# Kernel optimization log

Measured on AMD Instinct MI355X. Metric: run time of the kernel, lower is better.

The kernel has to match this reference:

```python
import jax, jax.numpy as jnp
import numpy as np

NUM_HEADS = 16
HEAD_DIM = 128
ROT_DIM = 128  # rotary_emb_dim == head_dim
ROPE_BASE = 10000.0


def setup_inputs() -> dict:
    key = jax.random.key(0)
    k1, k2, k3, k4, k5 = jax.random.split(key, 5)
    b, s, d = 2, 2048, 2048
    return {
        "x": jax.random.normal(k1, (b, s, d), jnp.float32),
        "Wqkv_w": jax.random.normal(k2, (3 * d, d), jnp.float32) * (d ** -0.5),
        "Wqkv_b": jax.random.normal(k3, (3 * d,), jnp.float32) * 0.02,
        "wo_w": jax.random.normal(k4, (d, d), jnp.float32) * (d ** -0.5),
        "wo_b": jax.random.normal(k5, (d,), jnp.float32) * 0.02,
    }


def _deinterleave(t):
    # torch.cat([t[..., ::2], t[..., 1::2]], dim=-1)
    return jnp.concatenate([t[..., ::2], t[..., 1::2]], axis=-1)


def _rope(t, cos, sin):
    # non-interleaved (GPT-NeoX style) rotary on first ROT_DIM dims; here ROT_DIM == head_dim
    half = ROT_DIM // 2
    x1, x2 = t[..., :half], t[..., half:ROT_DIM]
    # cos/sin: (s, half) -> broadcast over (b, s, h, half)
    c = cos[None, :, None, :]
    sn = sin[None, :, None, :]
    return jnp.concatenate([x1 * c - x2 * sn, x2 * c + x1 * sn], axis=-1)


def reference(x, Wqkv_w, Wqkv_b, wo_w, wo_b):
    b, s, d = x.shape
    h, hd = NUM_HEADS, HEAD_DIM
    # fused QKV projection, layout '(h three d)' per original rearrange
    qkv = x @ Wqkv_w.T + Wqkv_b                      # (b, s, 3*d)
    qkv = qkv.reshape(b, s, h, 3, hd)
    q = _deinterleave(qkv[:, :, :, 0, :])            # (b, s, h, hd)
    k = _deinterleave(qkv[:, :, :, 1, :])
    v = qkv[:, :, :, 2, :]
    # rotary embedding tables
    inv_freq = 1.0 / (ROPE_BASE ** (jnp.arange(0, ROT_DIM, 2, dtype=jnp.float32) / ROT_DIM))
    freqs = jnp.arange(s, dtype=jnp.float32)[:, None] * inv_freq[None, :]  # (s, half)
    cos, sin = jnp.cos(freqs), jnp.sin(freqs)
    q = _rope(q, cos, sin)
    k = _rope(k, cos, sin)
    # causal self-attention (SelfAttention, softmax_scale = 1/sqrt(hd))
    scale = hd ** -0.5
    scores = jnp.einsum('bshd,bthd->bhst', q, k) * scale  # (b, h, s, s)
    mask = jnp.tril(jnp.ones((s, s), dtype=bool))
    scores = jnp.where(mask[None, None], scores, jnp.finfo(scores.dtype).min)
    probs = jax.nn.softmax(scores, axis=-1)
    ctx = jnp.einsum('bhst,bthd->bshd', probs, v)    # (b, s, h, hd)
    ctx = ctx.reshape(b, s, d)
    return ctx @ wo_w.T + wo_b
```

## Files before the change

kernel.cpp:

```cpp
#include <hip/hip_runtime.h>

#define B_ 2
#define S_ 2048
#define H_ 16
#define HD_ 128
#define QKVROW 6144
#define M_ 4096

typedef float f32x4 __attribute__((ext_vector_type(4)));
typedef __bf16 bf16x8 __attribute__((ext_vector_type(8)));
typedef unsigned short ushortx8 __attribute__((ext_vector_type(8)));

__device__ __forceinline__ float bf2f(unsigned short u) {
  union { unsigned u; float f; } v;
  v.u = ((unsigned)u) << 16;
  return v.f;
}
__device__ __forceinline__ unsigned short f2bf(float f) {
  union { __bf16 b; unsigned short u; } c;
  c.b = (__bf16)f;
  return c.u;
}
__device__ __forceinline__ ushortx8 cvt8(const float* f) {
  const f32x4 lo = *(const f32x4*)f;
  const f32x4 hi = *(const f32x4*)(f + 4);
  ushortx8 o;
#pragma unroll
  for (int t = 0; t < 4; ++t) o[t] = f2bf(lo[t]);
#pragma unroll
  for (int t = 0; t < 4; ++t) o[4 + t] = f2bf(hi[t]);
  return o;
}
__device__ __forceinline__ void async16(const unsigned short* g, unsigned short* l) {
  __builtin_amdgcn_global_load_lds(
      (const __attribute__((address_space(1))) unsigned int*)g,
      (__attribute__((address_space(3))) unsigned int*)l, 16, 0, 0);
}

__global__ __launch_bounds__(256) void f2bf3t(
    const float* __restrict__ a, unsigned short* __restrict__ da, int na8,
    const float* __restrict__ b, unsigned short* __restrict__ db, int nb8,
    const float* __restrict__ c, unsigned short* __restrict__ dc, int nc8,
    float* __restrict__ tab, int nt8) {
  const int ntot = na8 + nb8 + nc8 + nt8;
  int i = blockIdx.x * 256 + threadIdx.x;
  const int stride = gridDim.x * 256;
  for (; i < ntot; i += stride) {
    int off = i;
    if (off < na8 + nb8 + nc8) {
      const float* s;
      unsigned short* d;
      if (off < na8) { s = a; d = da; }
      else if (off - na8 < nb8) { off -= na8; s = b; d = db; }
      else { off -= na8 + nb8; s = c; d = dc; }
      const ushortx8 o = cvt8(s + (size_t)off * 8);
      *(ushortx8*)&d[(size_t)off * 8] = o;
    } else {
      off -= na8 + nb8 + nc8;
      float* dt = tab + (size_t)off * 8;
      const int e0 = off * 8;
      const int s = e0 >> 7;
#pragma unroll
      for (int k = 0; k < 4; ++k) {
        const int j = ((e0 & 127) >> 1) + k;
        const float invf = expf(-(float)j * 0.14391156831212787f);
        float sn, cs;
        sincosf((float)s * invf, &sn, &cs);
        dt[2 * k] = cs;
        dt[2 * k + 1] = sn;
      }
    }
  }
}

__global__ __launch_bounds__(256) void gemm1(
    const unsigned short* __restrict__ A, const unsigned short* __restrict__ Bm,
    const float* __restrict__ bias, unsigned short* __restrict__ C) {
  __shared__ unsigned short As[128 * 64];
  __shared__ unsigned short Bs[128 * 64];
  const int tid = threadIdx.x;
  const int lane = tid & 63, wave = tid >> 6;
  const int l15 = lane & 15, quad = lane >> 4;
  const int m0 = blockIdx.y * 128, n0 = blockIdx.x * 128;
  const int wr = (wave >> 1) * 64, wc = (wave & 1) * 64;

  f32x4 acc[4][4];
#pragma unroll
  for (int r = 0; r < 4; ++r)
#pragma unroll
    for (int c = 0; c < 4; ++c) acc[r][c] = (f32x4){0.f, 0.f, 0.f, 0.f};

  for (int k0 = 0; k0 < 2048; k0 += 64) {
    __syncthreads();
#pragma unroll
    for (int i = 0; i < 4; ++i) {
      const int c0 = wave * 256 + i * 64;
      const int u = c0 + lane;
      const int row = u >> 3, cu = u & 7;
      const int cs = cu ^ (row & 7);
      async16(A + (size_t)(m0 + row) * 2048 + k0 + cs * 8, &As[c0 * 8]);
      async16(Bm + (size_t)(n0 + row) * 2048 + k0 + cs * 8, &Bs[c0 * 8]);
    }
    __syncthreads();

#pragma unroll
    for (int s = 0; s < 2; ++s) {
      bf16x8 af[4], bf[4];
#pragma unroll
      for (int r = 0; r < 4; ++r) {
        const int row = wr + r * 16 + l15;
        af[r] = *(const bf16x8*)&As[row * 64 + (((s * 4 + quad) ^ (row & 7)) << 3)];
      }
#pragma unroll
      for (int c = 0; c < 4; ++c) {
        const int row = wc + c * 16 + l15;
        bf[c] = *(const bf16x8*)&Bs[row * 64 + (((s * 4 + quad) ^ (row & 7)) << 3)];
      }
#pragma unroll
      for (int r = 0; r < 4; ++r)
#pragma unroll
        for (int c = 0; c < 4; ++c)
          acc[r][c] = __builtin_amdgcn_mfma_f32_16x16x32_bf16(af[r], bf[c], acc[r][c], 0, 0, 0);
    }
  }

#pragma unroll
  for (int c = 0; c < 4; ++c) {
    const int col = n0 + wc + c * 16 + l15;
    const float bv = bias[col];
#pragma unroll
    for (int r = 0; r < 4; ++r) {
      const int row = m0 + wr + r * 16 + quad * 4;
#pragma unroll
      for (int i = 0; i < 4; ++i)
        C[(size_t)(row + i) * QKVROW + col] = f2bf(acc[r][c][i] + bv);
    }
  }
}

__global__ __launch_bounds__(256) void rope_vt(
    unsigned short* qkv, unsigned short* __restrict__ Vt,
    const float* __restrict__ tab) {
  __shared__ unsigned short vs[64 * 136];
  const int b = blockIdx.z, h = blockIdx.y, s0 = blockIdx.x * 64;
  const int tid = threadIdx.x;
  const int r = tid >> 2, cpart = (tid & 3) * 32;
  const int s = s0 + r;
  unsigned short* base = qkv + (size_t)(b * S_ + s) * QKVROW + h * 384;
  const int j0 = cpart >> 1;

  ushortx8 ivq[4], ivk[4], ivv[4];
#pragma unroll
  for (int i = 0; i < 4; ++i) {
    ivq[i] = *(const ushortx8*)&base[cpart + i * 8];
    ivk[i] = *(const ushortx8*)&base[128 + cpart + i * 8];
    ivv[i] = *(const ushortx8*)&base[256 + cpart + i * 8];
  }

  float cs[16], sn[16];
  {
    const f32x4* tr = (const f32x4*)&tab[(size_t)s * 128 + j0 * 2];
#pragma unroll
    for (int t = 0; t < 8; ++t) {
      const f32x4 v = tr[t];
      cs[2 * t] = v[0]; sn[2 * t] = v[1];
      cs[2 * t + 1] = v[2]; sn[2 * t + 1] = v[3];
    }
  }

  __syncthreads();

#pragma unroll
  for (int which = 0; which < 2; ++which) {
    const ushortx8* iv = (which == 0) ? ivq : ivk;
    const float scale =
        (which == 0) ? (0.08838834764831845f * 1.4426950408889634f) : 1.0f;
    ushortx8 o1a, o1b, o2a, o2b;
#pragma unroll
    for (int t = 0; t < 16; ++t) {
      const float x1 = bf2f(iv[(2 * t) >> 3][(2 * t) & 7]);
      const float x2 = bf2f(iv[(2 * t + 1) >> 3][(2 * t + 1) & 7]);
      const unsigned short r1 = f2bf((x1 * cs[t] - x2 * sn[t]) * scale);
      const unsigned short r2 = f2bf((x2 * cs[t] + x1 * sn[t]) * scale);
      if (t < 8) { o1a[t] = r1; o2a[t] = r2; }
      else       { o1b[t - 8] = r1; o2b[t - 8] = r2; }
    }
    unsigned short* out = base + which * 128;
    *(ushortx8*)&out[j0] = o1a;
    *(ushortx8*)&out[j0 + 8] = o1b;
    *(ushortx8*)&out[64 + j0] = o2a;
    *(ushortx8*)&out[64 + j0 + 8] = o2b;
  }

#pragma unroll
  for (int i = 0; i < 4; ++i)
    *(ushortx8*)&vs[r * 136 + cpart + i * 8] = ivv[i];
  __syncthreads();
  const size_t vtb = (size_t)(b * H_ + h) * HD_ * S_ + s0;
#pragma unroll
  for (int it = 0; it < 4; ++it) {
    const int a = tid + it * 256;
    const int d = a >> 3, sc = (a & 7) * 8;
    ushortx8 o;
#pragma unroll
    for (int t = 0; t < 8; ++t) o[t] = vs[(sc + t) * 136 + d];
    *(ushortx8*)&Vt[vtb + (size_t)d * S_ + sc] = o;
  }
}

__global__ __launch_bounds__(256) void attn(
    unsigned short* qkv, const unsigned short* __restrict__ Vt) {
  __shared__ unsigned short Ks[64 * 128];
  __shared__ unsigned short Vs[128 * 64];
  __shared__ unsigned short Ps[4 * 16 * 64];
  const int bh = blockIdx.x, p = blockIdx.y, sub = blockIdx.z;
  const int b = bh >> 4, h = bh & 15;
  const int tid = threadIdx.x, lane = tid & 63, wave = tid >> 6;
  const int l15 = lane & 15, quad = lane >> 4;

  unsigned short* qh = qkv + (size_t)b * S_ * QKVROW + h * 384;
  const unsigned short* Vb = Vt + (size_t)bh * HD_ * S_;
  unsigned short* Pw = &Ps[wave * 16 * 64];

  ushortx8 rk[4], rv[4];
  auto pref = [&](int j) {
#pragma unroll
    for (int t = 0; t < 4; ++t) {
      const int uk = t * 256 + tid;
      const int krow = uk >> 4, kcu = uk & 15;
      rk[t] = *(const ushortx8*)(qh + (size_t)(j * 64 + krow) * QKVROW + 128 + kcu * 8);
      const int vrow = uk >> 3, vcu = uk & 7;
      rv[t] = *(const ushortx8*)(Vb + (size_t)vrow * S_ + j * 64 + vcu * 8);
    }
  };
  pref(0);

#pragma unroll
  for (int half = 0; half < 2; ++half) {
    const int qt = half ? 15 - p : p;
    const int jN = 2 * qt + 1 + sub;
    const int r0 = qt * 128 + sub * 64 + wave * 16;

    bf16x8 aq[4];
#pragma unroll
    for (int ks = 0; ks < 4; ++ks)
      aq[ks] = *(const bf16x8*)&qh[(size_t)(r0 + l15) * QKVROW + ks * 32 + quad * 8];

    f32x4 o[8];
    float mrow[4], lpart[4];
#pragma unroll
    for (int ct = 0; ct < 8; ++ct) o[ct] = (f32x4){0.f, 0.f, 0.f, 0.f};
#pragma unroll
    for (int i = 0; i < 4; ++i) { mrow[i] = -1e30f; lpart[i] = 0.f; }

    for (int j = 0; j < jN; ++j) {
      __syncthreads();
#pragma unroll
      for (int t = 0; t < 4; ++t) {
        const int uk = t * 256 + tid;
        const int krow = uk >> 4, kun = uk & 15;
        *(ushortx8*)&Ks[krow * 128 + ((kun ^ (krow & 7)) << 3)] = rk[t];
        const int vrow = uk >> 3, vun = uk & 7;
        *(ushortx8*)&Vs[vrow * 64 + ((vun ^ (vrow & 7)) << 3)] = rv[t];
      }
      __syncthreads();

      const int jn = (j + 1 < jN) ? j + 1 : (half == 0 ? 0 : -1);
      if (jn >= 0) pref(jn);

      f32x4 sacc[4];
#pragma unroll
      for (int ct = 0; ct < 4; ++ct) sacc[ct] = (f32x4){0.f, 0.f, 0.f, 0.f};
      __builtin_amdgcn_s_setprio(1);
#pragma unroll
      for (int ks = 0; ks < 4; ++ks) {
        bf16x8 bk[4];
#pragma unroll
        for (int ct = 0; ct < 4; ++ct)
          bk[ct] = *(const bf16x8*)&Ks[(ct * 16 + l15) * 128 +
                                       (((ks * 4 + quad) ^ (l15 & 7)) << 3)];
#pragma unroll
        for (int ct = 0; ct < 4; ++ct)
          sacc[ct] = __builtin_amdgcn_mfma_f32_16x16x32_bf16(aq[ks], bk[ct], sacc[ct], 0, 0, 0);
      }
      __builtin_amdgcn_s_setprio(0);

      if (j >= 2 * qt) {
#pragma unroll
        for (int ct = 0; ct < 4; ++ct)
#pragma unroll
          for (int i = 0; i < 4; ++i) {
            const int grow = r0 + quad * 4 + i;
            const int gcol = j * 64 + ct * 16 + l15;
            if (gcol > grow) sacc[ct][i] = -1e30f;
          }
      }

      float tmax[4];
#pragma unroll
      for (int i = 0; i < 4; ++i) {
        float m = fmaxf(fmaxf(sacc[0][i], sacc[1][i]), fmaxf(sacc[2][i], sacc[3][i]));
#pragma unroll
        for (int off = 1; off < 16; off <<= 1) m = fmaxf(m, __shfl_xor(m, off));
        tmax[i] = m;
      }
      bool need = false;
#pragma unroll
      for (int i = 0; i < 4; ++i) need = need || (tmax[i] > mrow[i] + 8.f);
      if (__any(need)) {
#pragma unroll
        for (int i = 0; i < 4; ++i) {
          const float mn = fmaxf(mrow[i], tmax[i]);
          const float alpha = exp2f(mrow[i] - mn);
          mrow[i] = mn;
          lpart[i] *= alpha;
#pragma unroll
          for (int ct = 0; ct < 8; ++ct) o[ct][i] *= alpha;
        }
      }
#pragma unroll
      for (int i = 0; i < 4; ++i) {
        float rs = 0.f;
#pragma unroll
        for (int ct = 0; ct < 4; ++ct) {
          const float pv = exp2f(sacc[ct][i] - mrow[i]);
          sacc[ct][i] = pv;
          rs += pv;
        }
        lpart[i] += rs;
      }

#pragma unroll
      for (int ct = 0; ct < 4; ++ct)
#pragma unroll
        for (int i = 0; i < 4; ++i) {
          const int row = quad * 4 + i;
          const int u = ct * 2 + (l15 >> 3);
          Pw[row * 64 + ((u ^ (row & 7)) << 3) + (l15 & 7)] = f2bf(sacc[ct][i]);
        }

      __builtin_amdgcn_s_setprio(1);
#pragma unroll
      for (int ks = 0; ks < 2; ++ks) {
        const bf16x8 ap = *(const bf16x8*)&Pw[l15 * 64 +
                                              (((ks * 4 + quad) ^ (l15 & 7)) << 3)];
        bf16x8 bv[8];
#pragma unroll
        for (int ct = 0; ct < 8; ++ct)
          bv[ct] = *(const bf16x8*)&Vs[(ct * 16 + l15) * 64 +
                                       (((ks * 4 + quad) ^ (l15 & 7)) << 3)];
#pragma unroll
        for (int ct = 0; ct < 8; ++ct)
          o[ct] = __builtin_amdgcn_mfma_f32_16x16x32_bf16(ap, bv[ct], o[ct], 0, 0, 0);
      }
      __builtin_amdgcn_s_setprio(0);
    }

    float inv[4];
#pragma unroll
    for (int i = 0; i < 4; ++i) {
      float l = lpart[i];
#pragma unroll
      for (int off = 1; off < 16; off <<= 1) l += __shfl_xor(l, off);
      inv[i] = 1.0f / l;
    }
#pragma unroll
    for (int ct = 0; ct < 8; ++ct)
#pragma unroll
      for (int i = 0; i < 4; ++i) {
        const int srow = r0 + quad * 4 + i;
        qh[(size_t)srow * QKVROW + ct * 16 + l15] = f2bf(o[ct][i] * inv[i]);
      }
  }
}

__global__ __launch_bounds__(256) void gemm2(
    const unsigned short* __restrict__ A, const unsigned short* __restrict__ Bm,
    const float* __restrict__ bias, float* __restrict__ C) {
  __shared__ unsigned short As[128 * 64];
  __shared__ unsigned short Bs[128 * 64];
  const int tid = threadIdx.x;
  const int lane = tid & 63, wave = tid >> 6;
  const int l15 = lane & 15, quad = lane >> 4;
  const int m0 = blockIdx.y * 128, n0 = blockIdx.x * 128;
  const int wr = (wave >> 1) * 64, wc = (wave & 1) * 64;

  f32x4 acc[4][4];
#pragma unroll
  for (int r = 0; r < 4; ++r)
#pragma unroll
    for (int c = 0; c < 4; ++c) acc[r][c] = (f32x4){0.f, 0.f, 0.f, 0.f};

  for (int k0 = 0; k0 < 2048; k0 += 64) {
    const int kh = ((k0 >> 7) * 384) + (k0 & 127);
    __syncthreads();
#pragma unroll
    for (int i = 0; i < 4; ++i) {
      const int c0 = wave * 256 + i * 64;
      const int u = c0 + lane;
      const int row = u >> 3, cu = u & 7;
      const int cs = cu ^ (row & 7);
      async16(A + (size_t)(m0 + row) * QKVROW + kh + cs * 8, &As[c0 * 8]);
      async16(Bm + (size_t)(n0 + row) * 2048 + k0 + cs * 8, &Bs[c0 * 8]);
    }
    __syncthreads();

#pragma unroll
    for (int s = 0; s < 2; ++s) {
      bf16x8 af[4], bf[4];
#pragma unroll
      for (int r = 0; r < 4; ++r) {
        const int row = wr + r * 16 + l15;
        af[r] = *(const bf16x8*)&As[row * 64 + (((s * 4 + quad) ^ (row & 7)) << 3)];
      }
#pragma unroll
      for (int c = 0; c < 4; ++c) {
        const int row = wc + c * 16 + l15;
        bf[c] = *(const bf16x8*)&Bs[row * 64 + (((s * 4 + quad) ^ (row & 7)) << 3)];
      }
#pragma unroll
      for (int r = 0; r < 4; ++r)
#pragma unroll
        for (int c = 0; c < 4; ++c)
          acc[r][c] = __builtin_amdgcn_mfma_f32_16x16x32_bf16(af[r], bf[c], acc[r][c], 0, 0, 0);
    }
  }

#pragma unroll
  for (int c = 0; c < 4; ++c) {
    const int col = n0 + wc + c * 16 + l15;
    const float bv = bias[col];
#pragma unroll
    for (int r = 0; r < 4; ++r) {
      const int row = m0 + wr + r * 16 + quad * 4;
#pragma unroll
      for (int i = 0; i < 4; ++i)
        C[(size_t)(row + i) * 2048 + col] = acc[r][c][i] + bv;
    }
  }
}

extern "C" void kernel_launch(void* const* d_in, const int* in_sizes, int n_in,
                              void* d_out, int out_size, void* d_ws, size_t ws_size,
                              hipStream_t stream) {
  const float* x    = (const float*)d_in[0];
  const float* wqkv = (const float*)d_in[1];
  const float* bqkv = (const float*)d_in[2];
  const float* wo   = (const float*)d_in[3];
  const float* bo   = (const float*)d_in[4];
  float* out = (float*)d_out;

  unsigned short* qkv = (unsigned short*)d_ws;
  unsigned short* Vt  = qkv + (size_t)M_ * QKVROW;
  unsigned short* xb  = Vt  + (size_t)B_ * H_ * HD_ * S_;
  unsigned short* wb  = xb  + (size_t)M_ * 2048;
  unsigned short* wob = wb  + (size_t)QKVROW * 2048;
  float* tab = (float*)(wob + (size_t)2048 * 2048);

  f2bf3t<<<dim3(2048), 256, 0, stream>>>(x, xb, (M_ * 2048) / 8,
                                         wqkv, wb, (QKVROW * 2048) / 8,
                                         wo, wob, (2048 * 2048) / 8,
                                         tab, (S_ * 128) / 8);

  gemm1<<<dim3(QKVROW / 128, M_ / 128), 256, 0, stream>>>(xb, wb, bqkv, qkv);
  rope_vt<<<dim3(S_ / 64, H_, B_), 256, 0, stream>>>(qkv, Vt, tab);
  attn<<<dim3(B_ * H_, 8, 2), 256, 0, stream>>>(qkv, Vt);
  gemm2<<<dim3(2048 / 128, M_ / 128), 256, 0, stream>>>(qkv, wob, bo, out);
}
```

Measured before the change: 405.0 us.

## Process two KV tiles per barrier round in causal attention loop

The attention inner loop now stages two 64-row K/V tiles into double-sized shared buffers per iteration and computes both before the next barrier pair. This halves the number of __syncthreads rounds and makes each prefetch batch larger, to cut synchronization and load-issue overhead. In exchange it doubles the K/V shared memory and the prefetch registers, which may lower occupancy. When the tile count is odd it also loads one extra tile that is never used.

```diff
diff --git a/kernel.cpp b/kernel.cpp
--- a/kernel.cpp
+++ b/kernel.cpp
@@ -210,8 +210,8 @@
 
 __global__ __launch_bounds__(256) void attn(
     unsigned short* qkv, const unsigned short* __restrict__ Vt) {
-  __shared__ unsigned short Ks[64 * 128];
-  __shared__ unsigned short Vs[128 * 64];
+  __shared__ unsigned short Ks[2][64 * 128];
+  __shared__ unsigned short Vs[2][128 * 64];
   __shared__ unsigned short Ps[4 * 16 * 64];
   const int bh = blockIdx.x, p = blockIdx.y, sub = blockIdx.z;
   const int b = bh >> 4, h = bh & 15;
@@ -222,15 +222,16 @@
   const unsigned short* Vb = Vt + (size_t)bh * HD_ * S_;
   unsigned short* Pw = &Ps[wave * 16 * 64];
 
-  ushortx8 rk[4], rv[4];
-  auto pref = [&](int j) {
-#pragma unroll
-    for (int t = 0; t < 4; ++t) {
-      const int uk = t * 256 + tid;
+  ushortx8 rk[8], rv[8];
+  auto pref = [&](int jp) {
+#pragma unroll
+    for (int t = 0; t < 8; ++t) {
+      const int tile = jp * 2 + (t >> 2);
+      const int uk = (t & 3) * 256 + tid;
       const int krow = uk >> 4, kcu = uk & 15;
-      rk[t] = *(const ushortx8*)(qh + (size_t)(j * 64 + krow) * QKVROW + 128 + kcu * 8);
+      rk[t] = *(const ushortx8*)(qh + (size_t)(tile * 64 + krow) * QKVROW + 128 + kcu * 8);
       const int vrow = uk >> 3, vcu = uk & 7;
-      rv[t] = *(const ushortx8*)(Vb + (size_t)vrow * S_ + j * 64 + vcu * 8);
+      rv[t] = *(const ushortx8*)(Vb + (size_t)vrow * S_ + tile * 64 + vcu * 8);
     }
   };
   pref(0);
@@ -239,6 +240,7 @@
   for (int half = 0; half < 2; ++half) {
     const int qt = half ? 15 - p : p;
     const int jN = 2 * qt + 1 + sub;
+    const int jP = (jN + 1) >> 1;
     const int r0 = qt * 128 + sub * 64 + wave * 16;
 
     bf16x8 aq[4];
@@ -253,107 +255,114 @@
 #pragma unroll
     for (int i = 0; i < 4; ++i) { mrow[i] = -1e30f; lpart[i] = 0.f; }
 
-    for (int j = 0; j < jN; ++j) {
+    for (int jp = 0; jp < jP; ++jp) {
       __syncthreads();
 #pragma unroll
-      for (int t = 0; t < 4; ++t) {
-        const int uk = t * 256 + tid;
+      for (int t = 0; t < 8; ++t) {
+        const int buf = t >> 2;
+        const int uk = (t & 3) * 256 + tid;
         const int krow = uk >> 4, kun = uk & 15;
-        *(ushortx8*)&Ks[krow * 128 + ((kun ^ (krow & 7)) << 3)] = rk[t];
+        *(ushortx8*)&Ks[buf][krow * 128 + ((kun ^ (krow & 7)) << 3)] = rk[t];
         const int vrow = uk >> 3, vun = uk & 7;
-        *(ushortx8*)&Vs[vrow * 64 + ((vun ^ (vrow & 7)) << 3)] = rv[t];
+        *(ushortx8*)&Vs[buf][vrow * 64 + ((vun ^ (vrow & 7)) << 3)] = rv[t];
       }
       __syncthreads();
 
-      const int jn = (j + 1 < jN) ? j + 1 : (half == 0 ? 0 : -1);
-      if (jn >= 0) pref(jn);
-
-      f32x4 sacc[4];
-#pragma unroll
-      for (int ct = 0; ct < 4; ++ct) sacc[ct] = (f32x4){0.f, 0.f, 0.f, 0.f};
-      __builtin_amdgcn_s_setprio(1);
-#pragma unroll
-      for (int ks = 0; ks < 4; ++ks) {
-        bf16x8 bk[4];
+      const int jpn = (jp + 1 < jP) ? jp + 1 : (half == 0 ? 0 : -1);
+      if (jpn >= 0) pref(jpn);
+
+#pragma unroll
+      for (int ht = 0; ht < 2; ++ht) {
+        const int j2 = jp * 2 + ht;
+        if (j2 >= jN) continue;
+
+        f32x4 sacc[4];
+#pragma unroll
+        for (int ct = 0; ct < 4; ++ct) sacc[ct] = (f32x4){0.f, 0.f, 0.f, 0.f};
+        __builtin_amdgcn_s_setprio(1);
+#pragma unroll
+        for (int ks = 0; ks < 4; ++ks) {
+          bf16x8 bk[4];
+#pragma unroll
+          for (int ct = 0; ct < 4; ++ct)
+            bk[ct] = *(const bf16x8*)&Ks[ht][(ct * 16 + l15) * 128 +
+                                            (((ks * 4 + quad) ^ (l15 & 7)) << 3)];
+#pragma unroll
+          for (int ct = 0; ct < 4; ++ct)
+            sacc[ct] = __builtin_amdgcn_mfma_f32_16x16x32_bf16(aq[ks], bk[ct], sacc[ct], 0, 0, 0);
+        }
+        __builtin_amdgcn_s_setprio(0);
+
+        if (j2 >= 2 * qt) {
+#pragma unroll
+          for (int ct = 0; ct < 4; ++ct)
+#pragma unroll
+            for (int i = 0; i < 4; ++i) {
+              const int grow = r0 + quad * 4 + i;
+              const int gcol = j2 * 64 + ct * 16 + l15;
+              if (gcol > grow) sacc[ct][i] = -1e30f;
+            }
+        }
+
+        float tmax[4];
+#pragma unroll
+        for (int i = 0; i < 4; ++i) {
+          float m = fmaxf(fmaxf(sacc[0][i], sacc[1][i]), fmaxf(sacc[2][i], sacc[3][i]));
+#pragma unroll
+          for (int off = 1; off < 16; off <<= 1) m = fmaxf(m, __shfl_xor(m, off));
+          tmax[i] = m;
+        }
+        bool need = false;
+#pragma unroll
+        for (int i = 0; i < 4; ++i) need = need || (tmax[i] > mrow[i] + 8.f);
+        if (__any(need)) {
+#pragma unroll
+          for (int i = 0; i < 4; ++i) {
+            const float mn = fmaxf(mrow[i], tmax[i]);
+            const float alpha = exp2f(mrow[i] - mn);
+            mrow[i] = mn;
+            lpart[i] *= alpha;
+#pragma unroll
+            for (int ct = 0; ct < 8; ++ct) o[ct][i] *= alpha;
+          }
+        }
+#pragma unroll
+        for (int i = 0; i < 4; ++i) {
+          float rs = 0.f;
+#pragma unroll
+          for (int ct = 0; ct < 4; ++ct) {
+            const float pv = exp2f(sacc[ct][i] - mrow[i]);
+            sacc[ct][i] = pv;
+            rs += pv;
+          }
+          lpart[i] += rs;
+        }
+
 #pragma unroll
         for (int ct = 0; ct < 4; ++ct)
-          bk[ct] = *(const bf16x8*)&Ks[(ct * 16 + l15) * 128 +
-                                       (((ks * 4 + quad) ^ (l15 & 7)) << 3)];
-#pragma unroll
-        for (int ct = 0; ct < 4; ++ct)
-          sacc[ct] = __builtin_amdgcn_mfma_f32_16x16x32_bf16(aq[ks], bk[ct], sacc[ct], 0, 0, 0);
-      }
-      __builtin_amdgcn_s_setprio(0);
-
-      if (j >= 2 * qt) {
-#pragma unroll
-        for (int ct = 0; ct < 4; ++ct)
 #pragma unroll
           for (int i = 0; i < 4; ++i) {
-            const int grow = r0 + quad * 4 + i;
-            const int gcol = j * 64 + ct * 16 + l15;
-            if (gcol > grow) sacc[ct][i] = -1e30f;
+            const int row = quad * 4 + i;
+            const int u = ct * 2 + (l15 >> 3);
+            Pw[row * 64 + ((u ^ (row & 7)) << 3) + (l15 & 7)] = f2bf(sacc[ct][i]);
           }
-      }
-
-      float tmax[4];
-#pragma unroll
-      for (int i = 0; i < 4; ++i) {
-        float m = fmaxf(fmaxf(sacc[0][i], sacc[1][i]), fmaxf(sacc[2][i], sacc[3][i]));
-#pragma unroll
-        for (int off = 1; off < 16; off <<= 1) m = fmaxf(m, __shfl_xor(m, off));
-        tmax[i] = m;
-      }
-      bool need = false;
-#pragma unroll
-      for (int i = 0; i < 4; ++i) need = need || (tmax[i] > mrow[i] + 8.f);
-      if (__any(need)) {
-#pragma unroll
-        for (int i = 0; i < 4; ++i) {
-          const float mn = fmaxf(mrow[i], tmax[i]);
-          const float alpha = exp2f(mrow[i] - mn);
-          mrow[i] = mn;
-          lpart[i] *= alpha;
-#pragma unroll
-          for (int ct = 0; ct < 8; ++ct) o[ct][i] *= alpha;
-        }
-      }
-#pragma unroll
-      for (int i = 0; i < 4; ++i) {
-        float rs = 0.f;
-#pragma unroll
-        for (int ct = 0; ct < 4; ++ct) {
-          const float pv = exp2f(sacc[ct][i] - mrow[i]);
-          sacc[ct][i] = pv;
-          rs += pv;
-        }
-        lpart[i] += rs;
-      }
-
-#pragma unroll
-      for (int ct = 0; ct < 4; ++ct)
-#pragma unroll
-        for (int i = 0; i < 4; ++i) {
-          const int row = quad * 4 + i;
-          const int u = ct * 2 + (l15 >> 3);
-          Pw[row * 64 + ((u ^ (row & 7)) << 3) + (l15 & 7)] = f2bf(sacc[ct][i]);
-        }
-
-      __builtin_amdgcn_s_setprio(1);
-#pragma unroll
-      for (int ks = 0; ks < 2; ++ks) {
-        const bf16x8 ap = *(const bf16x8*)&Pw[l15 * 64 +
-                                              (((ks * 4 + quad) ^ (l15 & 7)) << 3)];
-        bf16x8 bv[8];
-#pragma unroll
-        for (int ct = 0; ct < 8; ++ct)
-          bv[ct] = *(const bf16x8*)&Vs[(ct * 16 + l15) * 64 +
-                                       (((ks * 4 + quad) ^ (l15 & 7)) << 3)];
-#pragma unroll
-        for (int ct = 0; ct < 8; ++ct)
-          o[ct] = __builtin_amdgcn_mfma_f32_16x16x32_bf16(ap, bv[ct], o[ct], 0, 0, 0);
-      }
-      __builtin_amdgcn_s_setprio(0);
+
+        __builtin_amdgcn_s_setprio(1);
+#pragma unroll
+        for (int ks = 0; ks < 2; ++ks) {
+          const bf16x8 ap = *(const bf16x8*)&Pw[l15 * 64 +
+                                                (((ks * 4 + quad) ^ (l15 & 7)) << 3)];
+          bf16x8 bv[8];
+#pragma unroll
+          for (int ct = 0; ct < 8; ++ct)
+            bv[ct] = *(const bf16x8*)&Vs[ht][(ct * 16 + l15) * 64 +
+                                             (((ks * 4 + quad) ^ (l15 & 7)) << 3)];
+#pragma unroll
+          for (int ct = 0; ct < 8; ++ct)
+            o[ct] = __builtin_amdgcn_mfma_f32_16x16x32_bf16(ap, bv[ct], o[ct], 0, 0, 0);
+        }
+        __builtin_amdgcn_s_setprio(0);
+      }
     }
 
     float inv[4];
```

Result: slower. 450.0 us (+11.1%).
